# Optimization experiments

Measured on AMD Instinct MI355X. Metric: run time of the kernel, lower is better.

Reference implementation:

```python
import jax, jax.numpy as jnp
import numpy as np

EXP_CLAMP = 1.0e6
DENOM_EPS = 1e-10
LRELU_ALPHA = 0.01


def setup_inputs() -> dict:
    key = jax.random.key(0)
    k1, k2, k3, k4, k5, k6 = jax.random.split(key, 6)
    B, N, E, F = 4, 16384, 262144, 64
    h = jax.random.normal(k1, (B, N, F), dtype=jnp.float32)
    edge = jax.random.randint(k2, (B, E, 2), 0, N, dtype=jnp.int32)
    edge_num = jax.random.randint(k3, (B,), 1, E, dtype=jnp.int32)
    edge_weight = jax.random.uniform(k4, (B, E), dtype=jnp.float32)
    W = jax.random.normal(k5, (F, F), dtype=jnp.float32) * 0.15  # xavier-ish scale
    a = jax.random.normal(k6, (1, 2 * F), dtype=jnp.float32) * 0.12
    return {"h": h, "edge": edge, "edge_num": edge_num,
            "edge_weight": edge_weight, "W": W, "a": a}


def _seg_sum(src, idx, num_segments):
    # src: [E, ...], idx: [E] -> [num_segments, ...]
    return jax.ops.segment_sum(src, idx, num_segments=num_segments)


def reference(h, edge, edge_num, edge_weight, W, a):
    B, N, Fin = h.shape
    E = edge.shape[1]
    # linear transform: Wh = h @ W^T  -> [B, N, Fout]
    Wh = jnp.einsum('bnf,of->bno', h, W)
    ctr = edge[:, :, 0]  # [B, E]
    nbr = edge[:, :, 1]  # [B, E]
    Wh_c = jnp.take_along_axis(Wh, ctr[:, :, None], axis=1)  # [B, E, Fout]
    Wh_n = jnp.take_along_axis(Wh, nbr[:, :, None], axis=1)  # [B, E, Fout]
    a_input = jnp.concatenate([Wh_c, Wh_n], axis=-1) * edge_weight[:, :, None]
    # attention logits: leakyrelu(a_input @ a^T), squeeze to [B, E]
    att1 = jax.nn.leaky_relu(jnp.einsum('bek,k->be', a_input, a[0]), LRELU_ALPHA)
    # per-batch valid-edge mask (edges beyond edge_num zeroed, as in torch loop)
    mask = (jnp.arange(E, dtype=jnp.int32)[None, :] < edge_num[:, None])
    x_exp = jnp.clip(jnp.exp(att1), 0.0, EXP_CLAMP) * mask.astype(att1.dtype)
    # segment softmax denominator over center nodes
    denom = DENOM_EPS + jax.vmap(_seg_sum, in_axes=(0, 0, None))(x_exp, ctr, N)  # [B, N]
    att = x_exp / jnp.take_along_axis(denom, ctr, axis=1)  # [B, E]
    # weighted neighbor aggregation via scatter-add on center index
    att_Wh = Wh_n * att[:, :, None]  # masked edges already have att == 0
    h_prime = jax.vmap(_seg_sum, in_axes=(0, 0, None))(att_Wh, ctr, N)  # [B, N, Fout]
    return jax.nn.relu(h_prime)
```

## Files before the change

### kernel.cpp

```cpp
#include <hip/hip_runtime.h>

#define BB 4
#define NN 16384
#define EE 262144
#define FF 64
#define ROWS (BB * NN)
#define CAP 64

__device__ __forceinline__ unsigned short f32_to_bf16(float f) {
    unsigned int u = __float_as_uint(f);
    u += 0x7FFFu + ((u >> 16) & 1u);
    return (unsigned short)(u >> 16);
}

__global__ __launch_bounds__(256) void wh_kernel(
    const float* __restrict__ h, const float* __restrict__ W,
    const float* __restrict__ a,
    unsigned short* __restrict__ Wh, float* __restrict__ sc,
    float* __restrict__ sn, int* __restrict__ cnt)
{
    __shared__ float Wt[FF][68];
    __shared__ float hl[16][65];

    const int t = threadIdx.x;
    if (blockIdx.x < 256) cnt[blockIdx.x * 256 + t] = 0;

    for (int i = t; i < FF * FF; i += 256)
        Wt[i & 63][i >> 6] = W[i];
    const int rowBase = blockIdx.x * 16;
    {
        const float4* hp = (const float4*)(h + (size_t)rowBase * FF);
        float4 v = hp[t];
        int r = t >> 4, c = (t & 15) * 4;
        hl[r][c] = v.x; hl[r][c + 1] = v.y; hl[r][c + 2] = v.z; hl[r][c + 3] = v.w;
    }
    __syncthreads();

    const int r  = t >> 4;
    const int c4 = (t & 15) * 4;
    float4 acc = {0.f, 0.f, 0.f, 0.f};
    #pragma unroll
    for (int f = 0; f < FF; ++f) {
        const float hv = hl[r][f];
        const float4 w = *(const float4*)&Wt[f][c4];
        acc.x = fmaf(hv, w.x, acc.x);
        acc.y = fmaf(hv, w.y, acc.y);
        acc.z = fmaf(hv, w.z, acc.z);
        acc.w = fmaf(hv, w.w, acc.w);
    }
    const int row = rowBase + r;
    ushort4 st = { f32_to_bf16(acc.x), f32_to_bf16(acc.y),
                   f32_to_bf16(acc.z), f32_to_bf16(acc.w) };
    *(ushort4*)(Wh + (size_t)row * FF + c4) = st;

    float scv = acc.x * a[c4] + acc.y * a[c4 + 1] + acc.z * a[c4 + 2] + acc.w * a[c4 + 3];
    float snv = acc.x * a[FF + c4] + acc.y * a[FF + c4 + 1]
              + acc.z * a[FF + c4 + 2] + acc.w * a[FF + c4 + 3];
    #pragma unroll
    for (int off = 8; off; off >>= 1) {
        scv += __shfl_xor(scv, off);
        snv += __shfl_xor(snv, off);
    }
    if ((t & 15) == 0) { sc[row] = scv; sn[row] = snv; }
}

__global__ __launch_bounds__(256) void bin_kernel(
    const int* __restrict__ edge, const int* __restrict__ edge_num,
    const float* __restrict__ ew,
    const float* __restrict__ sc, const float* __restrict__ sn,
    int* __restrict__ cnt, unsigned int* __restrict__ payload)
{
    int idx = blockIdx.x * 256 + threadIdx.x;
    int b = idx >> 18, e = idx & (EE - 1);
    if (e >= edge_num[b]) return;
    int2 e2 = ((const int2*)edge)[idx];
    const int ctr = e2.x, nbr = e2.y;
    const int row = b * NN + ctr;
    float att1 = ew[idx] * (sc[row] + sn[b * NN + nbr]);
    att1 = att1 > 0.0f ? att1 : 0.01f * att1;
    float xe = fminf(__expf(att1), 1000000.0f);
    unsigned int u = __float_as_uint(xe);
    u = (u + 0x2000u) & 0xFFFFC000u;
    int pos = atomicAdd(&cnt[row], 1);
    if (pos < CAP)
        payload[(size_t)row * CAP + pos] = u | (unsigned int)nbr;
}

__global__ __launch_bounds__(256) void gather_kernel(
    const int* __restrict__ cnt, const unsigned int* __restrict__ payload,
    const uint2* __restrict__ Wh2,
    float* __restrict__ out)
{
    const int lane = threadIdx.x & 63;
    const int row = (blockIdx.x * 256 + threadIdx.x) >> 6;
    const int b = row >> 14;
    const int grp = lane >> 4;
    const int gl  = lane & 15;
    int deg = cnt[row];
    if (deg > CAP) deg = CAP;
    const unsigned int* pl = payload + (size_t)row * CAP;
    const uint2* WhB = Wh2 + (size_t)b * NN * 16;

    float a0 = 0.f, a1 = 0.f, a2 = 0.f, a3 = 0.f, dsum = 0.f;
    if (deg > 0) {
        const unsigned int p = (lane < deg) ? pl[lane] : 0u;
        for (int jj = 0; jj < deg; jj += 4) {
            const unsigned int pv = __shfl(p, jj + grp);
            const float xe = __uint_as_float(pv & 0xFFFFC000u);
            const int   n  = (int)(pv & 0x3FFFu);
            const uint2 w2 = WhB[(size_t)n * 16 + gl];
            a0 = fmaf(xe, __uint_as_float(w2.x << 16),        a0);
            a1 = fmaf(xe, __uint_as_float(w2.x & 0xFFFF0000u), a1);
            a2 = fmaf(xe, __uint_as_float(w2.y << 16),        a2);
            a3 = fmaf(xe, __uint_as_float(w2.y & 0xFFFF0000u), a3);
            dsum += xe;
        }
    }
    a0 += __shfl_xor(a0, 16); a1 += __shfl_xor(a1, 16);
    a2 += __shfl_xor(a2, 16); a3 += __shfl_xor(a3, 16);
    dsum += __shfl_xor(dsum, 16);
    a0 += __shfl_xor(a0, 32); a1 += __shfl_xor(a1, 32);
    a2 += __shfl_xor(a2, 32); a3 += __shfl_xor(a3, 32);
    dsum += __shfl_xor(dsum, 32);

    if (grp == 0) {
        const float inv = 1.0f / (1e-10f + dsum);
        float4 o;
        o.x = fmaxf(a0 * inv, 0.0f);
        o.y = fmaxf(a1 * inv, 0.0f);
        o.z = fmaxf(a2 * inv, 0.0f);
        o.w = fmaxf(a3 * inv, 0.0f);
        ((float4*)out)[(size_t)row * 16 + gl] = o;
    }
}

extern "C" void kernel_launch(void* const* d_in, const int* in_sizes, int n_in,
                              void* d_out, int out_size, void* d_ws, size_t ws_size,
                              hipStream_t stream)
{
    const float* h        = (const float*)d_in[0];
    const int*   edge     = (const int*)  d_in[1];
    const int*   edge_num = (const int*)  d_in[2];
    const float* ew       = (const float*)d_in[3];
    const float* W        = (const float*)d_in[4];
    const float* a        = (const float*)d_in[5];
    float* out = (float*)d_out;

    unsigned short* Wh = (unsigned short*)d_ws;
    float* sc        = (float*)(Wh + (size_t)BB * NN * FF);
    float* sn        = sc + ROWS;
    int*   cnt       = (int*)(sn + ROWS);
    unsigned int* payload = (unsigned int*)(cnt + ROWS);

    wh_kernel<<<ROWS / 16, 256, 0, stream>>>(h, W, a, Wh, sc, sn, cnt);

    bin_kernel<<<(BB * EE) / 256, 256, 0, stream>>>(edge, edge_num, ew, sc, sn,
                                                    cnt, payload);

    gather_kernel<<<ROWS / 4, 256, 0, stream>>>(cnt, payload,
                                                (const uint2*)Wh, out);
}
```

Measured before the change: 144.6 us.

## Fuse three kernels into one persistent kernel with software grid barriers

New measurement: 571.8 us. 295% more time.

```diff
diff --git a/kernel.cpp b/kernel.cpp
--- a/kernel.cpp
+++ b/kernel.cpp
@@ -6,6 +6,7 @@
 #define FF 64
 #define ROWS (BB * NN)
 #define CAP 64
+#define GRID 1024
 
 __device__ __forceinline__ unsigned short f32_to_bf16(float f) {
     unsigned int u = __float_as_uint(f);
@@ -13,124 +14,165 @@
     return (unsigned short)(u >> 16);
 }
 
-__global__ __launch_bounds__(256) void wh_kernel(
-    const float* __restrict__ h, const float* __restrict__ W,
-    const float* __restrict__ a,
+__device__ __forceinline__ void gsync(int* arrive, int* gen) {
+    __syncthreads();
+    if (threadIdx.x == 0) {
+        __threadfence();
+        int g = __hip_atomic_load(gen, __ATOMIC_ACQUIRE, __HIP_MEMORY_SCOPE_AGENT);
+        if (__hip_atomic_fetch_add(arrive, 1, __ATOMIC_ACQ_REL,
+                                   __HIP_MEMORY_SCOPE_AGENT) == GRID - 1) {
+            __hip_atomic_store(arrive, 0, __ATOMIC_RELAXED, __HIP_MEMORY_SCOPE_AGENT);
+            __hip_atomic_store(gen, g + 1, __ATOMIC_RELEASE, __HIP_MEMORY_SCOPE_AGENT);
+        } else {
+            int spins = 0;
+            while (__hip_atomic_load(gen, __ATOMIC_ACQUIRE,
+                                     __HIP_MEMORY_SCOPE_AGENT) == g) {
+                if (++spins > (1 << 26)) break;
+                __builtin_amdgcn_s_sleep(1);
+            }
+        }
+        __threadfence();
+    }
+    __syncthreads();
+}
+
+__global__ __launch_bounds__(256, 4) void fused_kernel(
+    const float* __restrict__ h, const int* __restrict__ edge,
+    const int* __restrict__ edge_num, const float* __restrict__ ew,
+    const float* __restrict__ W, const float* __restrict__ a,
     unsigned short* __restrict__ Wh, float* __restrict__ sc,
-    float* __restrict__ sn, int* __restrict__ cnt)
+    float* __restrict__ sn, int* __restrict__ cnt,
+    unsigned int* __restrict__ payload, float* __restrict__ out,
+    int* __restrict__ bar)
 {
     __shared__ float Wt[FF][68];
     __shared__ float hl[16][65];
 
     const int t = threadIdx.x;
-    if (blockIdx.x < 256) cnt[blockIdx.x * 256 + t] = 0;
+
+    for (int i = blockIdx.x * 256 + t; i < ROWS; i += GRID * 256)
+        cnt[i] = 0;
 
     for (int i = t; i < FF * FF; i += 256)
         Wt[i & 63][i >> 6] = W[i];
-    const int rowBase = blockIdx.x * 16;
-    {
-        const float4* hp = (const float4*)(h + (size_t)rowBase * FF);
-        float4 v = hp[t];
-        int r = t >> 4, c = (t & 15) * 4;
-        hl[r][c] = v.x; hl[r][c + 1] = v.y; hl[r][c + 2] = v.z; hl[r][c + 3] = v.w;
-    }
-    __syncthreads();
 
     const int r  = t >> 4;
     const int c4 = (t & 15) * 4;
-    float4 acc = {0.f, 0.f, 0.f, 0.f};
-    #pragma unroll
-    for (int f = 0; f < FF; ++f) {
-        const float hv = hl[r][f];
-        const float4 w = *(const float4*)&Wt[f][c4];
-        acc.x = fmaf(hv, w.x, acc.x);
-        acc.y = fmaf(hv, w.y, acc.y);
-        acc.z = fmaf(hv, w.z, acc.z);
-        acc.w = fmaf(hv, w.w, acc.w);
-    }
-    const int row = rowBase + r;
-    ushort4 st = { f32_to_bf16(acc.x), f32_to_bf16(acc.y),
-                   f32_to_bf16(acc.z), f32_to_bf16(acc.w) };
-    *(ushort4*)(Wh + (size_t)row * FF + c4) = st;
-
-    float scv = acc.x * a[c4] + acc.y * a[c4 + 1] + acc.z * a[c4 + 2] + acc.w * a[c4 + 3];
-    float snv = acc.x * a[FF + c4] + acc.y * a[FF + c4 + 1]
-              + acc.z * a[FF + c4 + 2] + acc.w * a[FF + c4 + 3];
-    #pragma unroll
-    for (int off = 8; off; off >>= 1) {
-        scv += __shfl_xor(scv, off);
-        snv += __shfl_xor(snv, off);
-    }
-    if ((t & 15) == 0) { sc[row] = scv; sn[row] = snv; }
-}
-
-__global__ __launch_bounds__(256) void bin_kernel(
-    const int* __restrict__ edge, const int* __restrict__ edge_num,
-    const float* __restrict__ ew,
-    const float* __restrict__ sc, const float* __restrict__ sn,
-    int* __restrict__ cnt, unsigned int* __restrict__ payload)
-{
-    int idx = blockIdx.x * 256 + threadIdx.x;
-    int b = idx >> 18, e = idx & (EE - 1);
-    if (e >= edge_num[b]) return;
-    int2 e2 = ((const int2*)edge)[idx];
-    const int ctr = e2.x, nbr = e2.y;
-    const int row = b * NN + ctr;
-    float att1 = ew[idx] * (sc[row] + sn[b * NN + nbr]);
-    att1 = att1 > 0.0f ? att1 : 0.01f * att1;
-    float xe = fminf(__expf(att1), 1000000.0f);
-    unsigned int u = __float_as_uint(xe);
-    u = (u + 0x2000u) & 0xFFFFC000u;
-    int pos = atomicAdd(&cnt[row], 1);
-    if (pos < CAP)
-        payload[(size_t)row * CAP + pos] = u | (unsigned int)nbr;
-}
-
-__global__ __launch_bounds__(256) void gather_kernel(
-    const int* __restrict__ cnt, const unsigned int* __restrict__ payload,
-    const uint2* __restrict__ Wh2,
-    float* __restrict__ out)
-{
-    const int lane = threadIdx.x & 63;
-    const int row = (blockIdx.x * 256 + threadIdx.x) >> 6;
-    const int b = row >> 14;
-    const int grp = lane >> 4;
-    const int gl  = lane & 15;
-    int deg = cnt[row];
-    if (deg > CAP) deg = CAP;
-    const unsigned int* pl = payload + (size_t)row * CAP;
-    const uint2* WhB = Wh2 + (size_t)b * NN * 16;
-
-    float a0 = 0.f, a1 = 0.f, a2 = 0.f, a3 = 0.f, dsum = 0.f;
-    if (deg > 0) {
+    for (int tile = blockIdx.x; tile < ROWS / 16; tile += GRID) {
+        const int rowBase = tile * 16;
+        __syncthreads();
+        {
+            const float4* hp = (const float4*)(h + (size_t)rowBase * FF);
+            float4 v = hp[t];
+            int rr = t >> 4, c = (t & 15) * 4;
+            hl[rr][c] = v.x; hl[rr][c + 1] = v.y; hl[rr][c + 2] = v.z; hl[rr][c + 3] = v.w;
+        }
+        __syncthreads();
+
+        float4 acc = {0.f, 0.f, 0.f, 0.f};
+        #pragma unroll
+        for (int f = 0; f < FF; ++f) {
+            const float hv = hl[r][f];
+            const float4 w = *(const float4*)&Wt[f][c4];
+            acc.x = fmaf(hv, w.x, acc.x);
+            acc.y = fmaf(hv, w.y, acc.y);
+            acc.z = fmaf(hv, w.z, acc.z);
+            acc.w = fmaf(hv, w.w, acc.w);
+        }
+        const int row = rowBase + r;
+        ushort4 st = { f32_to_bf16(acc.x), f32_to_bf16(acc.y),
+                       f32_to_bf16(acc.z), f32_to_bf16(acc.w) };
+        *(ushort4*)(Wh + (size_t)row * FF + c4) = st;
+
+        float scv = acc.x * a[c4] + acc.y * a[c4 + 1]
+                  + acc.z * a[c4 + 2] + acc.w * a[c4 + 3];
+        float snv = acc.x * a[FF + c4] + acc.y * a[FF + c4 + 1]
+                  + acc.z * a[FF + c4 + 2] + acc.w * a[FF + c4 + 3];
+        #pragma unroll
+        for (int off = 8; off; off >>= 1) {
+            scv += __shfl_xor(scv, off);
+            snv += __shfl_xor(snv, off);
+        }
+        if ((t & 15) == 0) { sc[row] = scv; sn[row] = snv; }
+    }
+
+    gsync(bar, bar + 1);
+
+    for (int i2 = blockIdx.x * 256 + t; i2 < (BB * EE) / 2; i2 += GRID * 256) {
+        const int b  = i2 >> 17;
+        const int e0 = (2 * i2) & (EE - 1);
+        const int en = edge_num[b];
+        const int4  e4 = ((const int4*)edge)[i2];
+        const float2 w2 = ((const float2*)ew)[i2];
+        #pragma unroll
+        for (int k = 0; k < 2; ++k) {
+            if (e0 + k >= en) continue;
+            const int ctr = k ? e4.z : e4.x;
+            const int nbr = k ? e4.w : e4.y;
+            const float wgt = k ? w2.y : w2.x;
+            const int row = b * NN + ctr;
+            float att1 = wgt * (sc[row] + sn[b * NN + nbr]);
+            att1 = att1 > 0.0f ? att1 : 0.01f * att1;
+            float xe = fminf(__expf(att1), 1000000.0f);
+            unsigned int u = __float_as_uint(xe);
+            u = (u + 0x2000u) & 0xFFFFC000u;
+            int pos = atomicAdd(&cnt[row], 1);
+            if (pos < CAP)
+                payload[(size_t)row * CAP + pos] = u | (unsigned int)nbr;
+        }
+    }
+
+    gsync(bar, bar + 1);
+
+    const int wave = t >> 6;
+    const int lane = t & 63;
+    const int grp  = lane >> 4;
+    const int gl   = lane & 15;
+    const uint2* Wh2 = (const uint2*)Wh;
+
+    for (int rg = blockIdx.x; rg < ROWS / 4; rg += GRID) {
+        const int row = rg * 4 + wave;
+        int deg = cnt[row];
+        if (deg > CAP) deg = CAP;
+        const unsigned int* pl = payload + (size_t)row * CAP;
+        const uint2* WhB = Wh2 + (size_t)(row >> 14) * NN * 16;
+
+        float a0 = 0.f, a1 = 0.f, a2 = 0.f, a3 = 0.f, dsum = 0.f;
         const unsigned int p = (lane < deg) ? pl[lane] : 0u;
-        for (int jj = 0; jj < deg; jj += 4) {
-            const unsigned int pv = __shfl(p, jj + grp);
-            const float xe = __uint_as_float(pv & 0xFFFFC000u);
-            const int   n  = (int)(pv & 0x3FFFu);
-            const uint2 w2 = WhB[(size_t)n * 16 + gl];
-            a0 = fmaf(xe, __uint_as_float(w2.x << 16),        a0);
-            a1 = fmaf(xe, __uint_as_float(w2.x & 0xFFFF0000u), a1);
-            a2 = fmaf(xe, __uint_as_float(w2.y << 16),        a2);
-            a3 = fmaf(xe, __uint_as_float(w2.y & 0xFFFF0000u), a3);
-            dsum += xe;
-        }
-    }
-    a0 += __shfl_xor(a0, 16); a1 += __shfl_xor(a1, 16);
-    a2 += __shfl_xor(a2, 16); a3 += __shfl_xor(a3, 16);
-    dsum += __shfl_xor(dsum, 16);
-    a0 += __shfl_xor(a0, 32); a1 += __shfl_xor(a1, 32);
-    a2 += __shfl_xor(a2, 32); a3 += __shfl_xor(a3, 32);
-    dsum += __shfl_xor(dsum, 32);
-
-    if (grp == 0) {
-        const float inv = 1.0f / (1e-10f + dsum);
-        float4 o;
-        o.x = fmaxf(a0 * inv, 0.0f);
-        o.y = fmaxf(a1 * inv, 0.0f);
-        o.z = fmaxf(a2 * inv, 0.0f);
-        o.w = fmaxf(a3 * inv, 0.0f);
-        ((float4*)out)[(size_t)row * 16 + gl] = o;
+        for (int jj = 0; jj < deg; jj += 8) {
+            const unsigned int pv0 = __shfl(p, jj + grp);
+            unsigned int pv1 = 0u;
+            if (jj + 4 < deg) pv1 = __shfl(p, jj + 4 + grp);
+            const float xe0 = __uint_as_float(pv0 & 0xFFFFC000u);
+            const float xe1 = __uint_as_float(pv1 & 0xFFFFC000u);
+            const uint2 w0 = WhB[(size_t)(pv0 & 0x3FFFu) * 16 + gl];
+            const uint2 w1 = WhB[(size_t)(pv1 & 0x3FFFu) * 16 + gl];
+            a0 = fmaf(xe0, __uint_as_float(w0.x << 16),         a0);
+            a1 = fmaf(xe0, __uint_as_float(w0.x & 0xFFFF0000u), a1);
+            a2 = fmaf(xe0, __uint_as_float(w0.y << 16),         a2);
+            a3 = fmaf(xe0, __uint_as_float(w0.y & 0xFFFF0000u), a3);
+            a0 = fmaf(xe1, __uint_as_float(w1.x << 16),         a0);
+            a1 = fmaf(xe1, __uint_as_float(w1.x & 0xFFFF0000u), a1);
+            a2 = fmaf(xe1, __uint_as_float(w1.y << 16),         a2);
+            a3 = fmaf(xe1, __uint_as_float(w1.y & 0xFFFF0000u), a3);
+            dsum += xe0 + xe1;
+        }
+        a0 += __shfl_xor(a0, 16); a1 += __shfl_xor(a1, 16);
+        a2 += __shfl_xor(a2, 16); a3 += __shfl_xor(a3, 16);
+        dsum += __shfl_xor(dsum, 16);
+        a0 += __shfl_xor(a0, 32); a1 += __shfl_xor(a1, 32);
+        a2 += __shfl_xor(a2, 32); a3 += __shfl_xor(a3, 32);
+        dsum += __shfl_xor(dsum, 32);
+
+        if (grp == 0) {
+            const float inv = 1.0f / (1e-10f + dsum);
+            float4 o;
+            o.x = fmaxf(a0 * inv, 0.0f);
+            o.y = fmaxf(a1 * inv, 0.0f);
+            o.z = fmaxf(a2 * inv, 0.0f);
+            o.w = fmaxf(a3 * inv, 0.0f);
+            ((float4*)out)[(size_t)row * 16 + gl] = o;
+        }
     }
 }
 
@@ -151,12 +193,10 @@
     float* sn        = sc + ROWS;
     int*   cnt       = (int*)(sn + ROWS);
     unsigned int* payload = (unsigned int*)(cnt + ROWS);
-
-    wh_kernel<<<ROWS / 16, 256, 0, stream>>>(h, W, a, Wh, sc, sn, cnt);
-
-    bin_kernel<<<(BB * EE) / 256, 256, 0, stream>>>(edge, edge_num, ew, sc, sn,
-                                                    cnt, payload);
-
-    gather_kernel<<<ROWS / 4, 256, 0, stream>>>(cnt, payload,
-                                                (const uint2*)Wh, out);
-}
+    int*   bar       = (int*)(payload + (size_t)ROWS * CAP);
+
+    hipMemsetAsync(bar, 0, 2 * sizeof(int), stream);
+
+    fused_kernel<<<GRID, 256, 0, stream>>>(h, edge, edge_num, ew, W, a,
+                                           Wh, sc, sn, cnt, payload, out, bar);
+}
```
